# Performance work log

Measured on AMD Instinct MI355X. Metric: run time of the kernel, lower is better.

Reference implementation:

```python
import jax, jax.numpy as jnp
import numpy as np
import math

EMBED = 1024
HEADS = 16
HEAD_DIM = EMBED // HEADS


def setup_inputs() -> dict:
    key = jax.random.key(0)
    ks = jax.random.split(key, 9)
    B, S = 2, 2048
    query = jax.random.normal(ks[0], (B, S, EMBED), dtype=jnp.float32)
    key_t = jax.random.normal(ks[1], (B, S, EMBED), dtype=jnp.float32)
    value = jax.random.normal(ks[2], (B, S, EMBED), dtype=jnp.float32)
    mask = jax.random.randint(ks[3], (B, 1, S, S), 0, 2, dtype=jnp.int32)
    # nn.Linear(head_dim, head_dim, bias=False) weights: [out, in]
    sc = 1.0 / math.sqrt(HEAD_DIM)
    Wq = jax.random.uniform(ks[4], (HEAD_DIM, HEAD_DIM), jnp.float32, -sc, sc)
    Wk = jax.random.uniform(ks[5], (HEAD_DIM, HEAD_DIM), jnp.float32, -sc, sc)
    Wv = jax.random.uniform(ks[6], (HEAD_DIM, HEAD_DIM), jnp.float32, -sc, sc)
    so = 1.0 / math.sqrt(EMBED)
    Wo = jax.random.uniform(ks[7], (EMBED, EMBED), jnp.float32, -so, so)
    bo = jax.random.uniform(ks[8], (EMBED,), jnp.float32, -so, so)
    return {"query": query, "key": key_t, "value": value, "mask": mask,
            "Wq": Wq, "Wk": Wk, "Wv": Wv, "Wo": Wo, "bo": bo}


def reference(query, key, value, mask, Wq, Wk, Wv, Wo, bo):
    B, Sq, E = query.shape
    Sk = key.shape[1]
    H, D = HEADS, HEAD_DIM
    # Faithful raw reshape into heads (as in the torch source, no transpose)
    q = query.reshape(B, H, Sq, D)
    k = key.reshape(B, H, Sk, D)
    v = value.reshape(B, H, Sk, D)
    # per-head_dim Linear (bias-free): x @ W.T
    Q = jnp.einsum('bhsd,ed->bhse', q, Wq)
    K = jnp.einsum('bhsd,ed->bhse', k, Wk)
    V = jnp.einsum('bhsd,ed->bhse', v, Wv)
    scores = jnp.einsum('bhqd,bhkd->bhqk', Q, K)  # [B,H,Sq,Sk]
    scores = jnp.where(mask == 0, jnp.float32(-1e20), scores)
    # NOTE: source divides by sqrt(embed_size), not sqrt(head_dim)
    attn = jax.nn.softmax(scores / jnp.float32(math.sqrt(E)), axis=-1)
    out = jnp.einsum('bhqk,bhkd->bhqd', attn, V).reshape(B, Sq, H * D)
    return out @ Wo.T + bo
```

## Files before the change

kernel.cpp:

```cpp
#include <hip/hip_runtime.h>

typedef __attribute__((ext_vector_type(8))) short short8;
typedef __attribute__((ext_vector_type(4))) float f32x4;
typedef __attribute__((ext_vector_type(2))) int int2v;
typedef __attribute__((ext_vector_type(4))) int int4v;

__device__ __forceinline__ short f2bf(float f) {
  unsigned u = __builtin_bit_cast(unsigned, f);
  u += 0x7fff + ((u >> 16) & 1);
  return (short)(u >> 16);
}

__device__ __forceinline__ int pk2bf(float lo, float hi) {
#if defined(__gfx950__) && __has_builtin(__builtin_amdgcn_cvt_pk_bf16_f32)
  typedef __attribute__((ext_vector_type(2))) __bf16 bf16x2;
  bf16x2 v = __builtin_amdgcn_cvt_pk_bf16_f32(lo, hi);
  return __builtin_bit_cast(int, v);
#else
  return (int)(unsigned short)(short)f2bf(lo) | (((int)f2bf(hi)) << 16);
#endif
}

__device__ __forceinline__ int pktr(float lo, float hi) {
  return (int)(__builtin_bit_cast(unsigned, lo) >> 16) |
         (int)(__builtin_bit_cast(unsigned, hi) & 0xffff0000u);
}

__device__ __forceinline__ short8 pack8(f32x4 a, f32x4 b) {
  int4v t;
  t.x = pk2bf(a[0], a[1]);
  t.y = pk2bf(a[2], a[3]);
  t.z = pk2bf(b[0], b[1]);
  t.w = pk2bf(b[2], b[3]);
  return __builtin_bit_cast(short8, t);
}

__device__ __forceinline__ float fand(float p, int m) {
  return __builtin_bit_cast(float, __builtin_bit_cast(int, p) & m);
}

__device__ __forceinline__ int bmask(unsigned w, int bit) {
#if __has_builtin(__builtin_amdgcn_sbfe)
  return __builtin_amdgcn_sbfe((int)w, bit, 1);
#else
  return ((int)(w << (31 - bit))) >> 31;
#endif
}

__device__ __forceinline__ float fexp2(float x) {
#if __has_builtin(__builtin_amdgcn_exp2f)
  return __builtin_amdgcn_exp2f(x);
#else
  return exp2f(x);
#endif
}

__device__ __forceinline__ void glds16(const short* g, short* lbase, int lane) {
#if __has_builtin(__builtin_amdgcn_global_load_lds)
  __builtin_amdgcn_global_load_lds(
      (const __attribute__((address_space(1))) unsigned int*)g,
      (__attribute__((address_space(3))) unsigned int*)lbase, 16, 0, 0);
#else
  *(short8*)(lbase + lane * 8) = *(const short8*)g;
#endif
}

__global__ __launch_bounds__(256) void prep(const float* __restrict__ q,
                                            const float* __restrict__ k,
                                            const float* __restrict__ v,
                                            const float* __restrict__ Wq,
                                            const float* __restrict__ Wk,
                                            const float* __restrict__ Wv,
                                            const float* __restrict__ Wo,
                                            const int* __restrict__ mask,
                                            short* __restrict__ Qp,
                                            short* __restrict__ Kp,
                                            short* __restrict__ Vtp,
                                            short* __restrict__ Wob,
                                            unsigned* __restrict__ mmod) {
  const int bid = blockIdx.x;
  const int tid = threadIdx.x;

  if (bid >= 4096) {
    const int mb = bid - 4096;
    const int kp = mb & 15, bq = mb >> 4;
    const int b_ = bq >> 5, q64 = bq & 31;
    const int wv = tid >> 6, qd = (tid >> 4) & 3, m16_ = tid & 15;
    unsigned d = 0;
#pragma unroll
    for (int hb = 0; hb < 2; ++hb) {
      const int ka = kp * 2 + hb;
#pragma unroll
      for (int r = 0; r < 4; ++r) {
        const int* mr = mask + b_ * 4194304 +
                        (q64 * 64 + wv * 16 + qd * 4 + r) * 2048 + ka * 64 + m16_;
#pragma unroll
        for (int nt = 0; nt < 4; ++nt)
          if (mr[nt * 16] != 0) d |= 1u << (hb * 16 + r * 4 + nt);
      }
    }
    mmod[mb * 256 + tid] = d;
    return;
  }
  if (bid >= 3072) {
    const int i = ((bid - 3072) * 256 + tid) * 4;
    const f32x4 x = *(const f32x4*)&Wo[i];
    int2v o;
    o.x = pk2bf(x[0], x[1]);
    o.y = pk2bf(x[2], x[3]);
    *(int2v*)&Wob[i] = o;
    return;
  }

  __shared__ short xt[64][72];
  __shared__ short ot[64][72];
  const int mode = bid >> 10;
  const int bt = bid & 1023;
  const float* X;
  const float* W;
  float scale;
  if (mode == 0) { X = q; W = Wq; scale = 0.045084220f; }
  else if (mode == 1) { X = k; W = Wk; scale = 1.0f; }
  else { X = v; W = Wv; scale = 1.0f; }

  const int r0 = bt * 64;
  const int row = tid >> 2, seg = (tid & 3) * 16;
  const f32x4* xs = (const f32x4*)(X + (r0 + row) * 64 + seg);
  const f32x4 x0 = xs[0], x1 = xs[1], x2 = xs[2], x3 = xs[3];
  *(short8*)&xt[row][seg] = pack8(x0, x1);
  *(short8*)&xt[row][seg + 8] = pack8(x2, x3);
  __syncthreads();

  const int lane = tid & 63, wave = tid >> 6;
  const int m16 = lane & 15, quad = lane >> 4;

  const short8 a0 = *(const short8*)&xt[wave * 16 + m16][quad * 8];
  const short8 a1 = *(const short8*)&xt[wave * 16 + m16][32 + quad * 8];

  f32x4 acc[4];
#pragma unroll
  for (int nt = 0; nt < 4; ++nt) {
    const f32x4* wp0 = (const f32x4*)&W[(nt * 16 + m16) * 64 + quad * 8];
    const f32x4* wp1 = (const f32x4*)&W[(nt * 16 + m16) * 64 + 32 + quad * 8];
    const short8 b0 = pack8(wp0[0], wp0[1]);
    const short8 b1 = pack8(wp1[0], wp1[1]);
    f32x4 z = (f32x4){0.f, 0.f, 0.f, 0.f};
    z = __builtin_amdgcn_mfma_f32_16x16x32_bf16(a0, b0, z, 0, 0, 0);
    z = __builtin_amdgcn_mfma_f32_16x16x32_bf16(a1, b1, z, 0, 0, 0);
    acc[nt] = z;
  }

  if (mode != 2) {
#pragma unroll
    for (int nt = 0; nt < 4; ++nt)
#pragma unroll
      for (int r = 0; r < 4; ++r)
        ot[wave * 16 + quad * 4 + r][nt * 16 + m16] = f2bf(acc[nt][r] * scale);
  } else {
#pragma unroll
    for (int nt = 0; nt < 4; ++nt)
#pragma unroll
      for (int r = 0; r < 4; ++r)
        ot[nt * 16 + m16][16 * quad + 4 * r + wave] = f2bf(acc[nt][r]);
  }
  __syncthreads();

  const int orow = tid >> 2, opart = tid & 3;
  if (mode != 2) {
    short* dst = (mode == 0 ? Qp : Kp) + (r0 + orow) * 64 + opart * 16;
    *(short8*)&dst[0] = *(const short8*)&ot[orow][opart * 16];
    *(short8*)&dst[8] = *(const short8*)&ot[orow][opart * 16 + 8];
  } else {
    const int bh = r0 >> 11, s0 = r0 & 2047;
    short* dst = Vtp + bh * 131072 + orow * 2048 + s0 + opart * 16;
    *(short8*)&dst[0] = *(const short8*)&ot[orow][opart * 16];
    *(short8*)&dst[8] = *(const short8*)&ot[orow][opart * 16 + 8];
  }
}

__global__ __launch_bounds__(256) void flash128(const short* __restrict__ Qp,
                                                const short* __restrict__ Kp,
                                                const short* __restrict__ Vt,
                                                const unsigned* __restrict__ mmod,
                                                short* __restrict__ Ob) {
  __shared__ __attribute__((aligned(16))) short kt0[4096];
  __shared__ __attribute__((aligned(16))) short kt1[4096];
  __shared__ __attribute__((aligned(16))) short vt0[4096];
  __shared__ __attribute__((aligned(16))) short vt1[4096];
  __shared__ __attribute__((aligned(16))) short pt[8192];
  const int tid = threadIdx.x;
  const int bid = blockIdx.x;
  const int local = bid >> 3;
  const int qblk = local & 15;
  const int bh = (bid & 7) * 4 + (local >> 4);
  const int q0 = qblk << 7;
  const int b = bh >> 4;
  const short* Qh = Qp + bh * 131072;
  const short* Kh = Kp + bh * 131072;
  const short* Vh = Vt + bh * 131072;
  const int lane = tid & 63, wave = tid >> 6;
  const int m16 = lane & 15, quad = lane >> 4;
  const int srow = lane >> 3, sj = (lane & 7) ^ srow;
  const int koff = m16 * 128 + ((quad ^ (m16 & 7)) * 16);
  const unsigned* mqa = mmod + ((b * 32 + qblk * 2) * 16) * 256 + tid;

  char* const ptB = (char*)pt;
  int woff[2][4];
  int aoff[2][2];
  const int aswz = (m16 & 7) << 4;
#pragma unroll
  for (int mi = 0; mi < 2; ++mi) {
#pragma unroll
    for (int r = 0; r < 4; ++r)
      woff[mi][r] = (mi * 64 + wave * 16 + quad * 4 + r) * 128 +
                    ((m16 * 8) ^ (((quad * 4 + r) & 7) << 4));
    aoff[mi][0] = (mi * 64 + wave * 16 + m16) * 128 + ((quad * 16) ^ aswz);
    aoff[mi][1] = (mi * 64 + wave * 16 + m16) * 128 + (((quad * 16) + 64) ^ aswz);
  }

  short8 aq[2][2];
#pragma unroll
  for (int mi = 0; mi < 2; ++mi)
#pragma unroll
    for (int h = 0; h < 2; ++h)
      aq[mi][h] = *(const short8*)&Qh[(q0 + mi * 64 + wave * 16 + m16) * 64 +
                                      h * 32 + quad * 8];

  float l[2][4] = {{0.f, 0.f, 0.f, 0.f}, {0.f, 0.f, 0.f, 0.f}};
  f32x4 oacc[2][4];
#pragma unroll
  for (int mi = 0; mi < 2; ++mi)
#pragma unroll
    for (int dt = 0; dt < 4; ++dt) oacc[mi][dt] = (f32x4){0.f, 0.f, 0.f, 0.f};

  auto stage = [&](short* ktb, short* vtb, int ka) {
#pragma unroll
    for (int t = 0; t < 2; ++t) {
      const int crow = wave * 16 + t * 8;
      glds16(Kh + (ka * 64 + crow + srow) * 64 + sj * 8, ktb + crow * 64, lane);
      glds16(Vh + (crow + srow) * 2048 + ka * 64 + sj * 8, vtb + crow * 64, lane);
    }
  };

  auto compute = [&](const short* ktp, const short* vtp, unsigned mwa, unsigned mwb,
                     int bitbase) {
    const char* ktb = (const char*)ktp;
    const char* vtb = (const char*)vtp;
    f32x4 s[2][4];
    __builtin_amdgcn_s_setprio(1);
#pragma unroll
    for (int nt = 0; nt < 4; ++nt) {
      const int o0 = nt * 2048 + koff;
      const short8 kb0 = *(const short8*)(ktb + o0);
      const short8 kb1 = *(const short8*)(ktb + (o0 ^ 64));
#pragma unroll
      for (int mi = 0; mi < 2; ++mi) {
        f32x4 z = (f32x4){0.f, 0.f, 0.f, 0.f};
        z = __builtin_amdgcn_mfma_f32_16x16x32_bf16(aq[mi][0], kb0, z, 0, 0, 0);
        z = __builtin_amdgcn_mfma_f32_16x16x32_bf16(aq[mi][1], kb1, z, 0, 0, 0);
        s[mi][nt] = z;
      }
    }
    __builtin_amdgcn_s_setprio(0);

#pragma unroll
    for (int mi = 0; mi < 2; ++mi) {
      const unsigned mw = mi ? mwb : mwa;
#pragma unroll
      for (int r = 0; r < 4; ++r) {
        float p[4];
#pragma unroll
        for (int nt = 0; nt < 4; ++nt)
          p[nt] = fand(fexp2(s[mi][nt][r]), bmask(mw, bitbase + r * 4 + nt));
        l[mi][r] += (p[0] + p[1]) + (p[2] + p[3]);
        int2v pp;
        pp.x = pktr(p[0], p[1]);
        pp.y = pktr(p[2], p[3]);
        *(int2v*)(ptB + woff[mi][r]) = pp;
      }
    }

    short8 ap[2][2];
#pragma unroll
    for (int mi = 0; mi < 2; ++mi) {
      ap[mi][0] = *(const short8*)(ptB + aoff[mi][0]);
      ap[mi][1] = *(const short8*)(ptB + aoff[mi][1]);
    }
    __builtin_amdgcn_s_setprio(1);
#pragma unroll
    for (int dt = 0; dt < 4; ++dt) {
      const int o0 = dt * 2048 + koff;
      const short8 vb0 = *(const short8*)(vtb + o0);
      const short8 vb1 = *(const short8*)(vtb + (o0 ^ 64));
#pragma unroll
      for (int mi = 0; mi < 2; ++mi) {
        f32x4 z = oacc[mi][dt];
        z = __builtin_amdgcn_mfma_f32_16x16x32_bf16(ap[mi][0], vb0, z, 0, 0, 0);
        z = __builtin_amdgcn_mfma_f32_16x16x32_bf16(ap[mi][1], vb1, z, 0, 0, 0);
        oacc[mi][dt] = z;
      }
    }
    __builtin_amdgcn_s_setprio(0);
  };

  unsigned mwa = mqa[0];
  unsigned mwb = mqa[4096];
  stage(kt0, vt0, 0);
  stage(kt1, vt1, 1);

  for (int kk = 0; kk < 15; ++kk) {
    const unsigned mwna = mqa[(kk + 1) * 256];
    const unsigned mwnb = mqa[4096 + (kk + 1) * 256];
    asm volatile("s_waitcnt vmcnt(6)" ::: "memory");
    __builtin_amdgcn_s_barrier();
    compute(kt0, vt0, mwa, mwb, 0);
    __builtin_amdgcn_s_barrier();
    stage(kt0, vt0, 2 * kk + 2);
    asm volatile("s_waitcnt vmcnt(6)" ::: "memory");
    __builtin_amdgcn_s_barrier();
    compute(kt1, vt1, mwa, mwb, 16);
    __builtin_amdgcn_s_barrier();
    stage(kt1, vt1, 2 * kk + 3);
    mwa = mwna;
    mwb = mwnb;
  }
  asm volatile("s_waitcnt vmcnt(4)" ::: "memory");
  __builtin_amdgcn_s_barrier();
  compute(kt0, vt0, mwa, mwb, 0);
  asm volatile("s_waitcnt vmcnt(0)" ::: "memory");
  __builtin_amdgcn_s_barrier();
  compute(kt1, vt1, mwa, mwb, 16);

#pragma unroll
  for (int mi = 0; mi < 2; ++mi)
#pragma unroll
    for (int r = 0; r < 4; ++r) {
#pragma unroll
      for (int off = 1; off < 16; off <<= 1) l[mi][r] += __shfl_xor(l[mi][r], off, 16);
      const float inv = 1.0f / l[mi][r];
#pragma unroll
      for (int dt = 0; dt < 4; ++dt)
        *(short*)(ptB + (mi * 64 + wave * 16 + quad * 4 + r) * 128 +
                  ((dt * 32 + m16 * 2) ^ (((quad * 4 + r) & 7) << 4))) =
            f2bf(oacc[mi][dt][r] * inv);
    }

  const int orow = lane >> 2, opart = lane & 3;
  const int oswz = (orow & 7) << 4;
#pragma unroll
  for (int mi = 0; mi < 2; ++mi) {
    const int prow = mi * 64 + wave * 16 + orow;
    short* og = Ob + (bh * 2048 + q0 + prow) * 64 + opart * 16;
    *(short8*)&og[0] = *(const short8*)(ptB + prow * 128 + ((opart * 32) ^ oswz));
    *(short8*)&og[8] = *(const short8*)(ptB + prow * 128 + ((opart * 32 + 16) ^ oswz));
  }
}

__global__ __launch_bounds__(256) void outproj(const short* __restrict__ Ob,
                                               const short* __restrict__ Wob,
                                               const float* __restrict__ bo,
                                               float* __restrict__ out) {
  __shared__ short at[64][72];
  __shared__ short bt[128][72];
  const int tid = threadIdx.x;
  const int bid = blockIdx.x;
  const int ct = bid >> 6, rt = bid & 63;
  const int r0 = rt * 64, c0 = ct * 128;
  const int lane = tid & 63, wave = tid >> 6;
  const int mr = (wave >> 1) * 32, nc = (wave & 1) * 64;
  const int m16 = lane & 15, quad = lane >> 4;
  const int arow = tid >> 2, apart = tid & 3;
  const int brow = tid >> 1, bhalf = (tid & 1) * 32;

  f32x4 acc[2][4];
#pragma unroll
  for (int mt = 0; mt < 2; ++mt)
#pragma unroll
    for (int nt = 0; nt < 4; ++nt) acc[mt][nt] = (f32x4){0.f, 0.f, 0.f, 0.f};

  for (int kc = 0; kc < 16; ++kc) {
    __syncthreads();
    const short* ag = &Ob[(r0 + arow) * 1024 + kc * 64 + apart * 16];
    const short* bg = &Wob[(c0 + brow) * 1024 + kc * 64 + bhalf];
    *(short8*)&at[arow][apart * 16] = *(const short8*)&ag[0];
    *(short8*)&at[arow][apart * 16 + 8] = *(const short8*)&ag[8];
    *(short8*)&bt[brow][bhalf] = *(const short8*)&bg[0];
    *(short8*)&bt[brow][bhalf + 8] = *(const short8*)&bg[8];
    *(short8*)&bt[brow][bhalf + 16] = *(const short8*)&bg[16];
    *(short8*)&bt[brow][bhalf + 24] = *(const short8*)&bg[24];
    __syncthreads();

#pragma unroll
    for (int kh = 0; kh < 2; ++kh) {
      short8 af[2], bf[4];
#pragma unroll
      for (int i = 0; i < 2; ++i)
        af[i] = *(const short8*)&at[mr + i * 16 + m16][kh * 32 + quad * 8];
#pragma unroll
      for (int j = 0; j < 4; ++j)
        bf[j] = *(const short8*)&bt[nc + j * 16 + m16][kh * 32 + quad * 8];
#pragma unroll
      for (int mt = 0; mt < 2; ++mt)
#pragma unroll
        for (int nt = 0; nt < 4; ++nt)
          acc[mt][nt] = __builtin_amdgcn_mfma_f32_16x16x32_bf16(af[mt], bf[nt], acc[mt][nt], 0, 0, 0);
    }
  }

#pragma unroll
  for (int nt = 0; nt < 4; ++nt) {
    const int col = c0 + nc + nt * 16 + m16;
    const float bias = bo[col];
#pragma unroll
    for (int mt = 0; mt < 2; ++mt)
#pragma unroll
      for (int rr2 = 0; rr2 < 4; ++rr2)
        out[(r0 + mr + mt * 16 + quad * 4 + rr2) * 1024 + col] = acc[mt][nt][rr2] + bias;
  }
}

extern "C" void kernel_launch(void* const* d_in, const int* in_sizes, int n_in,
                              void* d_out, int out_size, void* d_ws, size_t ws_size,
                              hipStream_t stream) {
  const float* query = (const float*)d_in[0];
  const float* key = (const float*)d_in[1];
  const float* value = (const float*)d_in[2];
  const int* mask = (const int*)d_in[3];
  const float* Wq = (const float*)d_in[4];
  const float* Wk = (const float*)d_in[5];
  const float* Wv = (const float*)d_in[6];
  const float* Wo = (const float*)d_in[7];
  const float* bo = (const float*)d_in[8];
  float* out = (float*)d_out;

  char* ws = (char*)d_ws;
  short* Qp = (short*)(ws);
  short* Kp = (short*)(ws + 8388608);
  short* Vt = (short*)(ws + 16777216);
  short* Ob = (short*)(ws + 25165824);
  short* Wob = (short*)(ws + 41943040);
  unsigned* mmod = (unsigned*)(ws + 44564480);

  prep<<<5120, 256, 0, stream>>>(query, key, value, Wq, Wk, Wv, Wo, mask,
                                 Qp, Kp, Vt, Wob, mmod);
  flash128<<<512, 256, 0, stream>>>(Qp, Kp, Vt, mmod, Ob);
  outproj<<<512, 256, 0, stream>>>(Ob, Wob, bo, out);
}
```

Measured before the change: 246.2 us.

## Split flash attention into 64-row query blocks with 2x2 wave split over queries and keys

Each flash block now handles 64 query rows instead of 128 and launches twice as many blocks. The four waves split as two query halves by two key-column halves. The P tile is shared through LDS, so each wave computes half the key columns of QK^T, and partial row sums are combined through LDS at the end. The aim is better CU occupancy and parallelism across the grid. In exchange, every K/V tile is loaded by twice as many blocks, and each tile step gains extra barriers and lgkmcnt waits between the QK and PV phases.

```diff
diff --git a/kernel.cpp b/kernel.cpp
--- a/kernel.cpp
+++ b/kernel.cpp
@@ -178,7 +178,7 @@
   }
 }
 
-__global__ __launch_bounds__(256) void flash128(const short* __restrict__ Qp,
+__global__ __launch_bounds__(256) void flash64s(const short* __restrict__ Qp,
                                                 const short* __restrict__ Kp,
                                                 const short* __restrict__ Vt,
                                                 const unsigned* __restrict__ mmod,
@@ -187,51 +187,56 @@
   __shared__ __attribute__((aligned(16))) short kt1[4096];
   __shared__ __attribute__((aligned(16))) short vt0[4096];
   __shared__ __attribute__((aligned(16))) short vt1[4096];
-  __shared__ __attribute__((aligned(16))) short pt[8192];
+  __shared__ __attribute__((aligned(16))) short pt[4096];
   const int tid = threadIdx.x;
   const int bid = blockIdx.x;
   const int local = bid >> 3;
-  const int qblk = local & 15;
-  const int bh = (bid & 7) * 4 + (local >> 4);
-  const int q0 = qblk << 7;
+  const int qblk = local & 31;
+  const int bh = (bid & 7) * 4 + (local >> 5);
+  const int q0 = qblk << 6;
   const int b = bh >> 4;
   const short* Qh = Qp + bh * 131072;
   const short* Kh = Kp + bh * 131072;
   const short* Vh = Vt + bh * 131072;
   const int lane = tid & 63, wave = tid >> 6;
+  const int qh = wave >> 1, kh = wave & 1;
   const int m16 = lane & 15, quad = lane >> 4;
   const int srow = lane >> 3, sj = (lane & 7) ^ srow;
   const int koff = m16 * 128 + ((quad ^ (m16 & 7)) * 16);
-  const unsigned* mqa = mmod + ((b * 32 + qblk * 2) * 16) * 256 + tid;
+  const int bbk = kh * 2;
+  const unsigned* mqp = mmod + ((b * 32 + qblk) * 16) * 256 + qh * 128 + quad * 16 + m16;
 
   char* const ptB = (char*)pt;
-  int woff[2][4];
-  int aoff[2][2];
-  const int aswz = (m16 & 7) << 4;
-#pragma unroll
-  for (int mi = 0; mi < 2; ++mi) {
-#pragma unroll
-    for (int r = 0; r < 4; ++r)
-      woff[mi][r] = (mi * 64 + wave * 16 + quad * 4 + r) * 128 +
-                    ((m16 * 8) ^ (((quad * 4 + r) & 7) << 4));
-    aoff[mi][0] = (mi * 64 + wave * 16 + m16) * 128 + ((quad * 16) ^ aswz);
-    aoff[mi][1] = (mi * 64 + wave * 16 + m16) * 128 + (((quad * 16) + 64) ^ aswz);
-  }
+  int pwoff[2][4];
+#pragma unroll
+  for (int mt = 0; mt < 2; ++mt)
+#pragma unroll
+    for (int r = 0; r < 4; ++r) {
+      const int row = qh * 32 + mt * 16 + quad * 4 + r;
+      pwoff[mt][r] = row * 128 + ((m16 * 8 + kh * 4) ^ ((row & 7) << 4));
+    }
+  int paoff[2][2];
+#pragma unroll
+  for (int mt = 0; mt < 2; ++mt)
+#pragma unroll
+    for (int h = 0; h < 2; ++h)
+      paoff[mt][h] = (qh * 32 + mt * 16 + m16) * 128 +
+                     ((quad * 16 + h * 64) ^ ((m16 & 7) << 4));
 
   short8 aq[2][2];
 #pragma unroll
-  for (int mi = 0; mi < 2; ++mi)
+  for (int mt = 0; mt < 2; ++mt)
 #pragma unroll
     for (int h = 0; h < 2; ++h)
-      aq[mi][h] = *(const short8*)&Qh[(q0 + mi * 64 + wave * 16 + m16) * 64 +
+      aq[mt][h] = *(const short8*)&Qh[(q0 + qh * 32 + mt * 16 + m16) * 64 +
                                       h * 32 + quad * 8];
 
   float l[2][4] = {{0.f, 0.f, 0.f, 0.f}, {0.f, 0.f, 0.f, 0.f}};
-  f32x4 oacc[2][4];
-#pragma unroll
-  for (int mi = 0; mi < 2; ++mi)
-#pragma unroll
-    for (int dt = 0; dt < 4; ++dt) oacc[mi][dt] = (f32x4){0.f, 0.f, 0.f, 0.f};
+  f32x4 oacc[2][2];
+#pragma unroll
+  for (int mt = 0; mt < 2; ++mt)
+#pragma unroll
+    for (int dt = 0; dt < 2; ++dt) oacc[mt][dt] = (f32x4){0.f, 0.f, 0.f, 0.f};
 
   auto stage = [&](short* ktb, short* vtb, int ka) {
 #pragma unroll
@@ -242,118 +247,145 @@
     }
   };
 
-  auto compute = [&](const short* ktp, const short* vtp, unsigned mwa, unsigned mwb,
-                     int bitbase) {
+  auto qk_phase = [&](const short* ktp, unsigned mw0, unsigned mw1, int bb) {
     const char* ktb = (const char*)ktp;
-    const char* vtb = (const char*)vtp;
-    f32x4 s[2][4];
+    f32x4 s[2][2];
     __builtin_amdgcn_s_setprio(1);
 #pragma unroll
-    for (int nt = 0; nt < 4; ++nt) {
-      const int o0 = nt * 2048 + koff;
+    for (int nt = 0; nt < 2; ++nt) {
+      const int o0 = (kh * 2 + nt) * 2048 + koff;
       const short8 kb0 = *(const short8*)(ktb + o0);
       const short8 kb1 = *(const short8*)(ktb + (o0 ^ 64));
 #pragma unroll
-      for (int mi = 0; mi < 2; ++mi) {
+      for (int mt = 0; mt < 2; ++mt) {
         f32x4 z = (f32x4){0.f, 0.f, 0.f, 0.f};
-        z = __builtin_amdgcn_mfma_f32_16x16x32_bf16(aq[mi][0], kb0, z, 0, 0, 0);
-        z = __builtin_amdgcn_mfma_f32_16x16x32_bf16(aq[mi][1], kb1, z, 0, 0, 0);
-        s[mi][nt] = z;
+        z = __builtin_amdgcn_mfma_f32_16x16x32_bf16(aq[mt][0], kb0, z, 0, 0, 0);
+        z = __builtin_amdgcn_mfma_f32_16x16x32_bf16(aq[mt][1], kb1, z, 0, 0, 0);
+        s[mt][nt] = z;
       }
     }
     __builtin_amdgcn_s_setprio(0);
-
-#pragma unroll
-    for (int mi = 0; mi < 2; ++mi) {
-      const unsigned mw = mi ? mwb : mwa;
+#pragma unroll
+    for (int mt = 0; mt < 2; ++mt) {
+      const unsigned mw = mt ? mw1 : mw0;
 #pragma unroll
       for (int r = 0; r < 4; ++r) {
-        float p[4];
-#pragma unroll
-        for (int nt = 0; nt < 4; ++nt)
-          p[nt] = fand(fexp2(s[mi][nt][r]), bmask(mw, bitbase + r * 4 + nt));
-        l[mi][r] += (p[0] + p[1]) + (p[2] + p[3]);
-        int2v pp;
-        pp.x = pktr(p[0], p[1]);
-        pp.y = pktr(p[2], p[3]);
-        *(int2v*)(ptB + woff[mi][r]) = pp;
+        const float p0 = fand(fexp2(s[0 + mt][0][r]), bmask(mw, bb + bbk + r * 4));
+        const float p1 = fand(fexp2(s[0 + mt][1][r]), bmask(mw, bb + bbk + r * 4 + 1));
+        l[mt][r] += p0 + p1;
+        *(int*)(ptB + pwoff[mt][r]) = pktr(p0, p1);
       }
     }
-
+  };
+
+  auto pv_phase = [&](const short* vtp) {
+    const char* vtb = (const char*)vtp;
     short8 ap[2][2];
 #pragma unroll
-    for (int mi = 0; mi < 2; ++mi) {
-      ap[mi][0] = *(const short8*)(ptB + aoff[mi][0]);
-      ap[mi][1] = *(const short8*)(ptB + aoff[mi][1]);
+    for (int mt = 0; mt < 2; ++mt) {
+      ap[mt][0] = *(const short8*)(ptB + paoff[mt][0]);
+      ap[mt][1] = *(const short8*)(ptB + paoff[mt][1]);
     }
     __builtin_amdgcn_s_setprio(1);
 #pragma unroll
-    for (int dt = 0; dt < 4; ++dt) {
-      const int o0 = dt * 2048 + koff;
+    for (int dt = 0; dt < 2; ++dt) {
+      const int o0 = (kh * 2 + dt) * 2048 + koff;
       const short8 vb0 = *(const short8*)(vtb + o0);
       const short8 vb1 = *(const short8*)(vtb + (o0 ^ 64));
 #pragma unroll
-      for (int mi = 0; mi < 2; ++mi) {
-        f32x4 z = oacc[mi][dt];
-        z = __builtin_amdgcn_mfma_f32_16x16x32_bf16(ap[mi][0], vb0, z, 0, 0, 0);
-        z = __builtin_amdgcn_mfma_f32_16x16x32_bf16(ap[mi][1], vb1, z, 0, 0, 0);
-        oacc[mi][dt] = z;
+      for (int mt = 0; mt < 2; ++mt) {
+        f32x4 z = oacc[mt][dt];
+        z = __builtin_amdgcn_mfma_f32_16x16x32_bf16(ap[mt][0], vb0, z, 0, 0, 0);
+        z = __builtin_amdgcn_mfma_f32_16x16x32_bf16(ap[mt][1], vb1, z, 0, 0, 0);
+        oacc[mt][dt] = z;
       }
     }
     __builtin_amdgcn_s_setprio(0);
   };
 
-  unsigned mwa = mqa[0];
-  unsigned mwb = mqa[4096];
+  unsigned mw0 = mqp[0];
+  unsigned mw1 = mqp[64];
   stage(kt0, vt0, 0);
   stage(kt1, vt1, 1);
 
   for (int kk = 0; kk < 15; ++kk) {
-    const unsigned mwna = mqa[(kk + 1) * 256];
-    const unsigned mwnb = mqa[4096 + (kk + 1) * 256];
+    const unsigned mwn0 = mqp[(kk + 1) * 256];
+    const unsigned mwn1 = mqp[(kk + 1) * 256 + 64];
     asm volatile("s_waitcnt vmcnt(6)" ::: "memory");
     __builtin_amdgcn_s_barrier();
-    compute(kt0, vt0, mwa, mwb, 0);
+    qk_phase(kt0, mw0, mw1, 0);
+    asm volatile("s_waitcnt lgkmcnt(0)" ::: "memory");
+    __builtin_amdgcn_s_barrier();
+    pv_phase(vt0);
+    asm volatile("s_waitcnt lgkmcnt(0)" ::: "memory");
     __builtin_amdgcn_s_barrier();
     stage(kt0, vt0, 2 * kk + 2);
     asm volatile("s_waitcnt vmcnt(6)" ::: "memory");
     __builtin_amdgcn_s_barrier();
-    compute(kt1, vt1, mwa, mwb, 16);
+    qk_phase(kt1, mw0, mw1, 16);
+    asm volatile("s_waitcnt lgkmcnt(0)" ::: "memory");
+    __builtin_amdgcn_s_barrier();
+    pv_phase(vt1);
+    asm volatile("s_waitcnt lgkmcnt(0)" ::: "memory");
     __builtin_amdgcn_s_barrier();
     stage(kt1, vt1, 2 * kk + 3);
-    mwa = mwna;
-    mwb = mwnb;
+    mw0 = mwn0;
+    mw1 = mwn1;
   }
   asm volatile("s_waitcnt vmcnt(4)" ::: "memory");
   __builtin_amdgcn_s_barrier();
-  compute(kt0, vt0, mwa, mwb, 0);
-  asm volatile("s_waitcnt vmcnt(0)" ::: "memory");
-  __builtin_amdgcn_s_barrier();
-  compute(kt1, vt1, mwa, mwb, 16);
-
-#pragma unroll
-  for (int mi = 0; mi < 2; ++mi)
+  qk_phase(kt0, mw0, mw1, 0);
+  asm volatile("s_waitcnt lgkmcnt(0)" ::: "memory");
+  __builtin_amdgcn_s_barrier();
+  pv_phase(vt0);
+  asm volatile("s_waitcnt lgkmcnt(0) vmcnt(0)" ::: "memory");
+  __builtin_amdgcn_s_barrier();
+  qk_phase(kt1, mw0, mw1, 16);
+  asm volatile("s_waitcnt lgkmcnt(0)" ::: "memory");
+  __builtin_amdgcn_s_barrier();
+  pv_phase(vt1);
+
+#pragma unroll
+  for (int mt = 0; mt < 2; ++mt)
+#pragma unroll
+    for (int r = 0; r < 4; ++r)
+#pragma unroll
+      for (int off = 1; off < 16; off <<= 1)
+        l[mt][r] += __shfl_xor(l[mt][r], off, 16);
+
+  float* lx = (float*)kt0;
+  if (m16 == 0) {
+#pragma unroll
+    for (int mt = 0; mt < 2; ++mt)
+#pragma unroll
+      for (int r = 0; r < 4; ++r)
+        lx[kh * 64 + qh * 32 + mt * 16 + quad * 4 + r] = l[mt][r];
+  }
+  asm volatile("s_waitcnt lgkmcnt(0)" ::: "memory");
+  __builtin_amdgcn_s_barrier();
+
+#pragma unroll
+  for (int mt = 0; mt < 2; ++mt)
 #pragma unroll
     for (int r = 0; r < 4; ++r) {
-#pragma unroll
-      for (int off = 1; off < 16; off <<= 1) l[mi][r] += __shfl_xor(l[mi][r], off, 16);
-      const float inv = 1.0f / l[mi][r];
-#pragma unroll
-      for (int dt = 0; dt < 4; ++dt)
-        *(short*)(ptB + (mi * 64 + wave * 16 + quad * 4 + r) * 128 +
-                  ((dt * 32 + m16 * 2) ^ (((quad * 4 + r) & 7) << 4))) =
-            f2bf(oacc[mi][dt][r] * inv);
-    }
+      const int row = qh * 32 + mt * 16 + quad * 4 + r;
+      const float lt = l[mt][r] + lx[(kh ^ 1) * 64 + row];
+      const float inv = 1.0f / lt;
+#pragma unroll
+      for (int dt = 0; dt < 2; ++dt)
+        *(short*)(ptB + row * 128 +
+                  ((kh * 64 + dt * 32 + m16 * 2) ^ ((row & 7) << 4))) =
+            f2bf(oacc[mt][dt][r] * inv);
+    }
+  asm volatile("s_waitcnt lgkmcnt(0)" ::: "memory");
+  __builtin_amdgcn_s_barrier();
 
   const int orow = lane >> 2, opart = lane & 3;
+  const int prow = wave * 16 + orow;
   const int oswz = (orow & 7) << 4;
-#pragma unroll
-  for (int mi = 0; mi < 2; ++mi) {
-    const int prow = mi * 64 + wave * 16 + orow;
-    short* og = Ob + (bh * 2048 + q0 + prow) * 64 + opart * 16;
-    *(short8*)&og[0] = *(const short8*)(ptB + prow * 128 + ((opart * 32) ^ oswz));
-    *(short8*)&og[8] = *(const short8*)(ptB + prow * 128 + ((opart * 32 + 16) ^ oswz));
-  }
+  short* og = Ob + (bh * 2048 + q0 + prow) * 64 + opart * 16;
+  *(short8*)&og[0] = *(const short8*)(ptB + prow * 128 + ((opart * 32) ^ oswz));
+  *(short8*)&og[8] = *(const short8*)(ptB + prow * 128 + ((opart * 32 + 16) ^ oswz));
 }
 
 __global__ __launch_bounds__(256) void outproj(const short* __restrict__ Ob,
@@ -443,6 +475,6 @@
 
   prep<<<5120, 256, 0, stream>>>(query, key, value, Wq, Wk, Wv, Wo, mask,
                                  Qp, Kp, Vt, Wob, mmod);
-  flash128<<<512, 256, 0, stream>>>(Qp, Kp, Vt, mmod, Ob);
+  flash64s<<<1024, 256, 0, stream>>>(Qp, Kp, Vt, mmod, Ob);
   outproj<<<512, 256, 0, stream>>>(Ob, Wob, bo, out);
 }
```

Measured after the change: 233.6 us. 5.1% less time.
